# Kernel tuning notes

Measured on AMD Instinct MI355X. Metric: run time of the kernel, lower is better.

## Reference

```python
import jax, jax.numpy as jnp
import numpy as np

N = 4_000_000          # total points
G = 100_000            # number of groups (patches)
PER = N // G           # equal group size (40) -> no empty groups
IN_DIM, MID_DIM, OUT_DIM = 5, 16, 16


def setup_inputs() -> dict:
    key = jax.random.key(0)
    k1, k2, k3, k4, k5 = jax.random.split(key, 5)
    data = jax.random.normal(k1, (N, IN_DIM), dtype=jnp.float32)
    # contiguous, non-decreasing group ids equivalent to torch.split(sizes) with
    # equal sizes of PER (deterministic 'sorted' ids; avoids empty groups which
    # would error in the original torch code).
    segment_ids = (jnp.arange(N, dtype=jnp.int32) // PER).astype(jnp.int32)
    W1 = jax.random.normal(k2, (IN_DIM, MID_DIM), dtype=jnp.float32) * (1.0 / np.sqrt(IN_DIM))
    b1 = jax.random.normal(k3, (MID_DIM,), dtype=jnp.float32) * 0.01
    W2 = jax.random.normal(k4, (MID_DIM, OUT_DIM), dtype=jnp.float32) * (1.0 / np.sqrt(MID_DIM))
    b2 = jax.random.normal(k5, (OUT_DIM,), dtype=jnp.float32) * 0.01
    return {"data": data, "segment_ids": segment_ids, "W1": W1, "b1": b1, "W2": W2, "b2": b2}


def reference(data, segment_ids, W1, b1, W2, b2):
    # 2-layer MLP: Linear -> ReLU -> Linear   (h: [N, OUT_DIM])
    h = jax.nn.relu(data @ W1 + b1) @ W2 + b2
    # ragged per-group max pooling (torch.split + per-group max, fused)
    out = jax.ops.segment_max(h, segment_ids, num_segments=G)  # [G, OUT_DIM]
    return out
```

## Files before the change

kernel.cpp:

```cpp
#include <hip/hip_runtime.h>


using bf16x8 = __attribute__((ext_vector_type(8))) short;
using f32x16 = __attribute__((ext_vector_type(16))) float;
using u32x4  = __attribute__((ext_vector_type(4))) unsigned int;

constexpr float SENT = -1.0e30f;

__device__ __forceinline__ unsigned packbf(float lo, float hi) {
    unsigned lu = __builtin_bit_cast(unsigned, lo) + 0x8000u;
    unsigned hu = __builtin_bit_cast(unsigned, hi) + 0x8000u;
    return (hu & 0xFFFF0000u) | (lu >> 16);
}

__global__ __launch_bounds__(256, 6)
void patch_mlp_max_mfma32c(const float* __restrict__ data,
                           const float* __restrict__ gW1, const float* __restrict__ gb1,
                           const float* __restrict__ gW2, const float* __restrict__ gb2,
                           float* __restrict__ out)
{
    const int tid  = threadIdx.x;
    const int lane = tid & 63;
    const int wid  = tid >> 6;
    const int m31  = lane & 31;
    const int h    = lane >> 5;

    float aw0 = 0.f, aw1 = 0.f, aw2 = 0.f;
    if (m31 < 16) {
        if (h == 0) { aw0 = gW1[0 * 16 + m31]; aw1 = gW1[1 * 16 + m31]; aw2 = gW1[2 * 16 + m31]; }
        else        { aw0 = gW1[3 * 16 + m31]; aw1 = gW1[4 * 16 + m31]; aw2 = gb1[m31]; }
    }
    u32x4 a1u = {packbf(aw0, aw1), packbf(aw2, 0.f), 0u, 0u};
    const bf16x8 a1 = __builtin_bit_cast(bf16x8, a1u);

    const int c  = lane & 15;
    const int k0 = h * 4;
    u32x4 b2u = {packbf(gW2[(k0 + 0)  * 16 + c], gW2[(k0 + 1)  * 16 + c]),
                 packbf(gW2[(k0 + 2)  * 16 + c], gW2[(k0 + 3)  * 16 + c]),
                 packbf(gW2[(k0 + 8)  * 16 + c], gW2[(k0 + 9)  * 16 + c]),
                 packbf(gW2[(k0 + 10) * 16 + c], gW2[(k0 + 11) * 16 + c])};
    const bf16x8 b2f = __builtin_bit_cast(bf16x8, b2u);
    const float  b2v = gb2[c];

    const f32x16 zero16 = {0.f, 0.f, 0.f, 0.f, 0.f, 0.f, 0.f, 0.f,
                           0.f, 0.f, 0.f, 0.f, 0.f, 0.f, 0.f, 0.f};

    const int    gbase = (blockIdx.x * 4 + wid) * 8;
    const float* base  = data + (size_t)gbase * 200;

    const int voA = m31 * 5 + (h ? 3 : 0);
    const int voC = voA + 2 - h;

    float acc[8];
    #pragma unroll
    for (int g = 0; g < 8; ++g) acc[g] = SENT;

    #pragma unroll
    for (int s = 0; s < 10; ++s) {
        const int sb = s * 160;
        const float v0  = base[voA + sb];
        const float v1  = base[voA + sb + 1];
        const float v2l = base[voC + sb];
        const float v2  = h ? 1.0f : v2l;

        u32x4 bxu = {packbf(v0, v1), packbf(v2, 0.f), 0u, 0u};
        f32x16 d1 = __builtin_amdgcn_mfma_f32_32x32x16_bf16(
            a1, __builtin_bit_cast(bf16x8, bxu), zero16, 0, 0, 0);

        u32x4 a2u = {packbf(fmaxf(d1[0], 0.f), fmaxf(d1[1], 0.f)),
                     packbf(fmaxf(d1[2], 0.f), fmaxf(d1[3], 0.f)),
                     packbf(fmaxf(d1[4], 0.f), fmaxf(d1[5], 0.f)),
                     packbf(fmaxf(d1[6], 0.f), fmaxf(d1[7], 0.f))};
        f32x16 d2 = __builtin_amdgcn_mfma_f32_32x32x16_bf16(
            __builtin_bit_cast(bf16x8, a2u), b2f, zero16, 0, 0, 0);

        #pragma unroll
        for (int r = 0; r < 16; ++r) {
            const int g = (32 * s + (r & 3) + 8 * (r >> 2)) / 40;
            acc[g] = fmaxf(acc[g], d2[r]);
        }
    }

    #pragma unroll
    for (int g = 0; g < 8; ++g)
        acc[g] = fmaxf(acc[g], __shfl_xor(acc[g], 32, 64));

    if (lane < 16) {
        #pragma unroll
        for (int g = 0; g < 8; ++g)
            out[(size_t)(gbase + g) * 16 + lane] = acc[g] + b2v;
    }
}

extern "C" void kernel_launch(void* const* d_in, const int* in_sizes, int n_in,
                              void* d_out, int out_size, void* d_ws, size_t ws_size,
                              hipStream_t stream) {
    const float* data = (const float*)d_in[0];
    const float* W1 = (const float*)d_in[2];
    const float* b1 = (const float*)d_in[3];
    const float* W2 = (const float*)d_in[4];
    const float* b2 = (const float*)d_in[5];
    float* out = (float*)d_out;

    dim3 grid(3125), block(256);
    patch_mlp_max_mfma32c<<<grid, block, 0, stream>>>(data, W1, b1, W2, b2, out);
}
```

Measured before the change: 22.03 us.

## Process 64 points per first-layer MFMA by packing all 5 inputs per lane

Each lane now loads all five input features of its own point, so one 32x32x16 MFMA computes layer one for 64 points: the two 32-column blocks of the output hold separate point sets. The W1 A-operand is laid out to match. The layer-one MFMA count is halved (5 per wave instead of 10), and each of the two output halves feeds its own layer-two MFMA. Each lane loads more scalars per iteration and the per-lane load pattern changes. The aim is fewer MFMA and packing instructions in a kernel that is likely memory-bound.

```diff
diff --git a/kernel.cpp b/kernel.cpp
--- a/kernel.cpp
+++ b/kernel.cpp
@@ -14,10 +14,10 @@
 }
 
 __global__ __launch_bounds__(256, 6)
-void patch_mlp_max_mfma32c(const float* __restrict__ data,
-                           const float* __restrict__ gW1, const float* __restrict__ gb1,
-                           const float* __restrict__ gW2, const float* __restrict__ gb2,
-                           float* __restrict__ out)
+void patch_mlp_max_mfma64(const float* __restrict__ data,
+                          const float* __restrict__ gW1, const float* __restrict__ gb1,
+                          const float* __restrict__ gW2, const float* __restrict__ gb2,
+                          float* __restrict__ out)
 {
     const int tid  = threadIdx.x;
     const int lane = tid & 63;
@@ -25,12 +25,14 @@
     const int m31  = lane & 31;
     const int h    = lane >> 5;
 
-    float aw0 = 0.f, aw1 = 0.f, aw2 = 0.f;
-    if (m31 < 16) {
-        if (h == 0) { aw0 = gW1[0 * 16 + m31]; aw1 = gW1[1 * 16 + m31]; aw2 = gW1[2 * 16 + m31]; }
-        else        { aw0 = gW1[3 * 16 + m31]; aw1 = gW1[4 * 16 + m31]; aw2 = gb1[m31]; }
+    const bool wlane = (lane < 16) || (lane >= 48);
+    const int  wi    = lane & 15;
+    u32x4 a1u = {0u, 0u, 0u, 0u};
+    if (wlane) {
+        a1u.x = packbf(gW1[0 * 16 + wi], gW1[1 * 16 + wi]);
+        a1u.y = packbf(gW1[2 * 16 + wi], gW1[3 * 16 + wi]);
+        a1u.z = packbf(gW1[4 * 16 + wi], gb1[wi]);
     }
-    u32x4 a1u = {packbf(aw0, aw1), packbf(aw2, 0.f), 0u, 0u};
     const bf16x8 a1 = __builtin_bit_cast(bf16x8, a1u);
 
     const int c  = lane & 15;
@@ -48,36 +50,48 @@
     const int    gbase = (blockIdx.x * 4 + wid) * 8;
     const float* base  = data + (size_t)gbase * 200;
 
-    const int voA = m31 * 5 + (h ? 3 : 0);
-    const int voC = voA + 2 - h;
+    const int vo = (m31 + 32 * h) * 5;
 
     float acc[8];
     #pragma unroll
     for (int g = 0; g < 8; ++g) acc[g] = SENT;
 
     #pragma unroll
-    for (int s = 0; s < 10; ++s) {
-        const int sb = s * 160;
-        const float v0  = base[voA + sb];
-        const float v1  = base[voA + sb + 1];
-        const float v2l = base[voC + sb];
-        const float v2  = h ? 1.0f : v2l;
+    for (int s = 0; s < 5; ++s) {
+        const int sb = s * 320;
+        const float x0 = base[vo + sb];
+        const float x1 = base[vo + sb + 1];
+        const float x2 = base[vo + sb + 2];
+        const float x3 = base[vo + sb + 3];
+        const float x4 = base[vo + sb + 4];
 
-        u32x4 bxu = {packbf(v0, v1), packbf(v2, 0.f), 0u, 0u};
+        u32x4 bxu = {packbf(x0, x1), packbf(x2, x3), packbf(x4, 1.0f), 0u};
         f32x16 d1 = __builtin_amdgcn_mfma_f32_32x32x16_bf16(
             a1, __builtin_bit_cast(bf16x8, bxu), zero16, 0, 0, 0);
 
-        u32x4 a2u = {packbf(fmaxf(d1[0], 0.f), fmaxf(d1[1], 0.f)),
-                     packbf(fmaxf(d1[2], 0.f), fmaxf(d1[3], 0.f)),
-                     packbf(fmaxf(d1[4], 0.f), fmaxf(d1[5], 0.f)),
-                     packbf(fmaxf(d1[6], 0.f), fmaxf(d1[7], 0.f))};
-        f32x16 d2 = __builtin_amdgcn_mfma_f32_32x32x16_bf16(
-            __builtin_bit_cast(bf16x8, a2u), b2f, zero16, 0, 0, 0);
+        u32x4 a2a = {packbf(fmaxf(d1[0],  0.f), fmaxf(d1[1],  0.f)),
+                     packbf(fmaxf(d1[2],  0.f), fmaxf(d1[3],  0.f)),
+                     packbf(fmaxf(d1[4],  0.f), fmaxf(d1[5],  0.f)),
+                     packbf(fmaxf(d1[6],  0.f), fmaxf(d1[7],  0.f))};
+        u32x4 a2b = {packbf(fmaxf(d1[8],  0.f), fmaxf(d1[9],  0.f)),
+                     packbf(fmaxf(d1[10], 0.f), fmaxf(d1[11], 0.f)),
+                     packbf(fmaxf(d1[12], 0.f), fmaxf(d1[13], 0.f)),
+                     packbf(fmaxf(d1[14], 0.f), fmaxf(d1[15], 0.f))};
 
+        f32x16 d2a = __builtin_amdgcn_mfma_f32_32x32x16_bf16(
+            __builtin_bit_cast(bf16x8, a2a), b2f, zero16, 0, 0, 0);
         #pragma unroll
         for (int r = 0; r < 16; ++r) {
-            const int g = (32 * s + (r & 3) + 8 * (r >> 2)) / 40;
-            acc[g] = fmaxf(acc[g], d2[r]);
+            const int g = (64 * s + (r & 3) + 8 * (r >> 2)) / 40;
+            acc[g] = fmaxf(acc[g], d2a[r]);
+        }
+
+        f32x16 d2b = __builtin_amdgcn_mfma_f32_32x32x16_bf16(
+            __builtin_bit_cast(bf16x8, a2b), b2f, zero16, 0, 0, 0);
+        #pragma unroll
+        for (int r = 0; r < 16; ++r) {
+            const int g = (64 * s + 32 + (r & 3) + 8 * (r >> 2)) / 40;
+            acc[g] = fmaxf(acc[g], d2b[r]);
         }
     }
 
@@ -103,5 +117,5 @@
     float* out = (float*)d_out;
 
     dim3 grid(3125), block(256);
-    patch_mlp_max_mfma32c<<<grid, block, 0, stream>>>(data, W1, b1, W2, b2, out);
+    patch_mlp_max_mfma64<<<grid, block, 0, stream>>>(data, W1, b1, W2, b2, out);
 }
```

Result: no change. 22.09 us (+0.3%).
